# Kernel optimization log

Measured on AMD Instinct MI355X. Metric: run time of the kernel, lower is better.

## Reference

```python
import jax, jax.numpy as jnp
import numpy as np

N = 50000
E = 800000
EP = 200000
IN_C = 128
HID = 128


def setup_inputs() -> dict:
    key = jax.random.key(0)
    ks = jax.random.split(key, 10)
    x = jax.random.normal(ks[0], (N, IN_C), dtype=jnp.float32)
    edge_index = jax.random.randint(ks[1], (2, E), 0, N, dtype=jnp.int64)
    pred_edges = jax.random.randint(ks[2], (2, EP), 0, N, dtype=jnp.int64)
    s_in = 1.0 / np.sqrt(IN_C)
    s_h = 1.0 / np.sqrt(HID)
    W1l = jax.random.normal(ks[3], (IN_C, HID), dtype=jnp.float32) * s_in
    W1r = jax.random.normal(ks[4], (IN_C, HID), dtype=jnp.float32) * s_in
    b1 = jnp.zeros((HID,), dtype=jnp.float32)
    W2l = jax.random.normal(ks[5], (HID, HID), dtype=jnp.float32) * s_h
    W2r = jax.random.normal(ks[6], (HID, HID), dtype=jnp.float32) * s_h
    b2 = jnp.zeros((HID,), dtype=jnp.float32)
    return {"x": x, "W1l": W1l, "b1": b1, "W1r": W1r,
            "W2l": W2l, "b2": b2, "W2r": W2r,
            "edge_index": edge_index, "pred_edges": pred_edges}


def _sage_conv(h, Wl, b, Wr, src, dst, n_nodes):
    # PyG SAGEConv (aggr='mean'): out = lin_l(mean_j x_j) + lin_r(x_i)
    msg = h[src]                                              # (E, D) gather
    agg = jax.ops.segment_sum(msg, dst, num_segments=n_nodes)  # (N, D) scatter-add
    deg = jax.ops.segment_sum(jnp.ones((src.shape[0],), h.dtype), dst,
                              num_segments=n_nodes)
    agg = agg / jnp.maximum(deg, 1.0)[:, None]                # mean (0 for isolated)
    return agg @ Wl + b + h @ Wr


def reference(x, W1l, b1, W1r, W2l, b2, W2r, edge_index, pred_edges):
    n_nodes = x.shape[0]
    src, dst = edge_index[0], edge_index[1]
    h = jax.nn.relu(_sage_conv(x, W1l, b1, W1r, src, dst, n_nodes))
    z = _sage_conv(h, W2l, b2, W2r, src, dst, n_nodes)
    ps, pd = pred_edges[0], pred_edges[1]
    return jnp.sum(z[ps] * z[pd], axis=-1)  # (E_pred,) logits
```

## Files before the change

### kernel.cpp

```cpp
#include <hip/hip_runtime.h>

#define D 128

typedef __attribute__((ext_vector_type(8))) short short8;
typedef __attribute__((ext_vector_type(4))) float f32x4;

__device__ inline unsigned int f2bf_bits(float f) {
    unsigned int u = __float_as_uint(f);
    return (u + 0x7FFFu + ((u >> 16) & 1u)) >> 16;
}

__device__ inline float bfhi(unsigned int u) { return __uint_as_float(u << 16); }
__device__ inline float bflo(unsigned int u) { return __uint_as_float(u & 0xffff0000u); }

__global__ __launch_bounds__(256) void prep_kernel(
    const float* __restrict__ x,
    const float* __restrict__ W1l, const float* __restrict__ W1r,
    const float* __restrict__ W2l, const float* __restrict__ W2r,
    unsigned short* __restrict__ xbf, unsigned short* __restrict__ xlo,
    unsigned short* __restrict__ h1, unsigned short* __restrict__ l1,
    unsigned short* __restrict__ h2, unsigned short* __restrict__ l2,
    int n4, int ncast, int* __restrict__ chist, int* __restrict__ csrpad)
{
    const int b = blockIdx.x;
    const int t = threadIdx.x;
    if (b < ncast) {
        int i = b * 256 + t;
        if (i >= n4) return;
        f32x4 v = *(const f32x4*)(x + (size_t)i * 4);
        ushort4 oh, ol;
        {
            unsigned int h; float hf;
            h = f2bf_bits(v.x); hf = __uint_as_float(h << 16);
            oh.x = (unsigned short)h; ol.x = (unsigned short)f2bf_bits(v.x - hf);
            h = f2bf_bits(v.y); hf = __uint_as_float(h << 16);
            oh.y = (unsigned short)h; ol.y = (unsigned short)f2bf_bits(v.y - hf);
            h = f2bf_bits(v.z); hf = __uint_as_float(h << 16);
            oh.z = (unsigned short)h; ol.z = (unsigned short)f2bf_bits(v.z - hf);
            h = f2bf_bits(v.w); hf = __uint_as_float(h << 16);
            oh.w = (unsigned short)h; ol.w = (unsigned short)f2bf_bits(v.w - hf);
        }
        *(ushort4*)(xbf + (size_t)i * 4) = oh;
        *(ushort4*)(xlo + (size_t)i * 4) = ol;
    } else if (b < ncast + 256) {
        int gidx = (b - ncast) * 256 + t;
        int sel = gidx >> 15;
        int idx = gidx & 32767;
        int tt = idx >> 12;
        int ks = (idx >> 9) & 7;
        int lane = (idx >> 3) & 63;
        int j = idx & 7;
        int qq = lane >> 4, r16 = lane & 15;
        int k = ks * 32 + qq * 8 + j;
        int c = tt * 16 + r16;
        const float* Wl = sel ? W2l : W1l;
        const float* Wr = sel ? W2r : W1r;
        float v = (k < 128) ? Wl[k * 128 + c] : Wr[(k - 128) * 128 + c];
        unsigned int h = f2bf_bits(v);
        float hf = __uint_as_float(h << 16);
        unsigned int l = f2bf_bits(v - hf);
        (sel ? h2 : h1)[idx] = (unsigned short)h;
        (sel ? l2 : l1)[idx] = (unsigned short)l;
    } else {
        chist[t] = 0;
        if (t < 16) csrpad[t] = 0;
    }
}

__global__ __launch_bounds__(256) void coarse_count_kernel(const int* __restrict__ dst,
                                                           int* __restrict__ chist, int E) {
    __shared__ int h[256];
    h[threadIdx.x] = 0;
    __syncthreads();
    const int stride = gridDim.x * 256;
    for (int e = blockIdx.x * 256 + threadIdx.x; e < E; e += stride)
        atomicAdd(&h[dst[e] >> 8], 1);
    __syncthreads();
    int v = h[threadIdx.x];
    if (v) atomicAdd(&chist[threadIdx.x], v);
}

__global__ __launch_bounds__(256) void scan256_kernel(const int* __restrict__ chist,
                                                      int* __restrict__ cbase,
                                                      int* __restrict__ gcur) {
    __shared__ int wsum[4];
    const int t = threadIdx.x, lane = t & 63, wv = t >> 6;
    int v = chist[t];
    int s = v;
#pragma unroll
    for (int o = 1; o < 64; o <<= 1) {
        int u = __shfl_up(s, o, 64);
        if (lane >= o) s += u;
    }
    if (lane == 63) wsum[wv] = s;
    __syncthreads();
    int add = 0;
    for (int w = 0; w < wv; ++w) add += wsum[w];
    cbase[t + 1] = s + add;
    if (t == 0) cbase[0] = 0;
    gcur[t] = s + add - v;
}

#define CCHUNK 4096
__global__ __launch_bounds__(256) void coarse_scatter_kernel(
    const int* __restrict__ src, const int* __restrict__ dst,
    int* __restrict__ gcur, unsigned int* __restrict__ centries, int E)
{
    __shared__ int h[256];
    __shared__ int base[256];
    __shared__ unsigned int stage[CCHUNK];
    const int t = threadIdx.x;
    const int e0 = blockIdx.x * CCHUNK;
    h[t] = 0;
    __syncthreads();
#pragma unroll
    for (int i = 0; i < 16; ++i) {
        int e = e0 + i * 256 + t;
        unsigned int u = 0xFFFFFFFFu;
        if (e < E) {
            int d = dst[e];
            int s = src[e];
            int b = d >> 8;
            u = ((unsigned)b << 24) | ((unsigned)s << 8) | (unsigned)(d & 255);
            atomicAdd(&h[b], 1);
        }
        stage[i * 256 + t] = u;
    }
    __syncthreads();
    base[t] = atomicAdd(&gcur[t], h[t]);
    __syncthreads();
    h[t] = 0;
    __syncthreads();
#pragma unroll
    for (int i = 0; i < 16; ++i) {
        unsigned int u = stage[i * 256 + t];
        if (u != 0xFFFFFFFFu) {
            int b = u >> 24;
            int r = atomicAdd(&h[b], 1);
            centries[base[b] + r] = u & 0x00FFFFFFu;
        }
    }
}

#define DCAP 8192
__global__ __launch_bounds__(256) void fine_bucket_kernel(
    const unsigned int* __restrict__ centries,
    const int* __restrict__ cbase,
    int* __restrict__ offo, int* __restrict__ csr, int N, int E)
{
    __shared__ int h[256], ex[256], wsum[4];
    __shared__ int stg[DCAP];
    const int t = threadIdx.x, lane = t & 63, wv = t >> 6;
    const int b = blockIdx.x;
    const int s0 = cbase[b];
    const int cnt = cbase[b + 1] - s0;
    h[t] = 0;
    __syncthreads();
    for (int i = t; i < cnt; i += 256)
        atomicAdd(&h[centries[s0 + i] & 255], 1);
    __syncthreads();
    int v = h[t], s = v;
#pragma unroll
    for (int o = 1; o < 64; o <<= 1) {
        int u = __shfl_up(s, o, 64);
        if (lane >= o) s += u;
    }
    if (lane == 63) wsum[wv] = s;
    __syncthreads();
    int add = 0;
    for (int w = 0; w < wv; ++w) add += wsum[w];
    const int exc = s + add - v;
    ex[t] = exc;
    const int dg = b * 256 + t;
    if (dg < N) offo[dg] = s0 + exc;
    if (b == 0 && t == 0) offo[N] = E;
    h[t] = 0;
    __syncthreads();
    if (cnt <= DCAP) {
        for (int i = t; i < cnt; i += 256) {
            unsigned int u = centries[s0 + i];
            int dl = u & 255;
            int r = atomicAdd(&h[dl], 1);
            stg[ex[dl] + r] = (int)(u >> 8);
        }
        __syncthreads();
        for (int i = t; i < cnt; i += 256)
            csr[s0 + i] = stg[i];
    } else {
        for (int i = t; i < cnt; i += 256) {
            unsigned int u = centries[s0 + i];
            int dl = u & 255;
            int r = atomicAdd(&h[dl], 1);
            csr[s0 + ex[dl] + r] = (int)(u >> 8);
        }
    }
}

__device__ inline void loadb8(const unsigned short* __restrict__ bh,
                              const unsigned short* __restrict__ bl,
                              int ks, short8* BH, short8* BL) {
    const unsigned short* p = bh + (size_t)ks * 512;
    const unsigned short* q = bl + (size_t)ks * 512;
#pragma unroll
    for (int t = 0; t < 8; ++t) {
        BH[t] = *(const short8*)(p + (size_t)t * 4096);
        BL[t] = *(const short8*)(q + (size_t)t * 4096);
    }
}

__device__ inline void mfma24(const short8& AH, const short8& AL,
                              const short8* BH, const short8* BL, f32x4* acc) {
#pragma unroll
    for (int t = 0; t < 8; ++t) {
        acc[t] = __builtin_amdgcn_mfma_f32_16x16x32_bf16(AH, BH[t], acc[t], 0, 0, 0);
        acc[t] = __builtin_amdgcn_mfma_f32_16x16x32_bf16(AL, BH[t], acc[t], 0, 0, 0);
        acc[t] = __builtin_amdgcn_mfma_f32_16x16x32_bf16(AH, BL[t], acc[t], 0, 0, 0);
    }
}

__global__ __launch_bounds__(64, 3) void fused_sage_kernel(
    const unsigned short* __restrict__ featbf,
    const int* __restrict__ off,
    const int* __restrict__ csr,
    const unsigned short* __restrict__ self_hi,
    const unsigned short* __restrict__ self_lo,
    const unsigned short* __restrict__ wpk_hi,
    const unsigned short* __restrict__ wpk_lo,
    const float* __restrict__ bias,
    unsigned short* __restrict__ out_hi,
    unsigned short* __restrict__ out_lo,
    int do_relu)
{
    const int lane = threadIdx.x;
    const int tile = blockIdx.x;
    const int q = lane >> 4, r16 = lane & 15;
    const int n0w = tile * 16;
    const int node = n0w + r16;

    const unsigned short* bh = wpk_hi + lane * 8;
    const unsigned short* bl = wpk_lo + lane * 8;

    short8 BH0[8], BL0[8], BH1[8], BL1[8];
    loadb8(bh, bl, 0, BH0, BL0);

    const int start = off[node];
    const int end   = off[node + 1];
    const unsigned short* fb = featbf + q * 8;
    float ga[4][8];
#pragma unroll
    for (int k = 0; k < 4; ++k)
#pragma unroll
        for (int c = 0; c < 8; ++c) ga[k][c] = 0.f;

#define ACCUM(rv, k)                                                     \
    { ga[k][0] += bfhi(rv.x); ga[k][1] += bflo(rv.x);                    \
      ga[k][2] += bfhi(rv.y); ga[k][3] += bflo(rv.y);                    \
      ga[k][4] += bfhi(rv.z); ga[k][5] += bflo(rv.z);                    \
      ga[k][6] += bfhi(rv.w); ga[k][7] += bflo(rv.w); }

    const uint4 zero4 = {0u, 0u, 0u, 0u};
    if (start < end) {
        int4 ix = *(const int4*)(csr + start);
        for (int e = start; e < end; e += 4) {
            int4 ixn = *(const int4*)(csr + e + 4);
            const unsigned short* p0 = fb + (size_t)ix.x * D;
            const unsigned short* p1 = fb + (size_t)ix.y * D;
            const unsigned short* p2 = fb + (size_t)ix.z * D;
            const unsigned short* p3 = fb + (size_t)ix.w * D;
            uint4 r00 = *(const uint4*)(p0);
            uint4 r01 = *(const uint4*)(p0 + 32);
            uint4 r02 = *(const uint4*)(p0 + 64);
            uint4 r03 = *(const uint4*)(p0 + 96);
            uint4 r10 = *(const uint4*)(p1);
            uint4 r11 = *(const uint4*)(p1 + 32);
            uint4 r12 = *(const uint4*)(p1 + 64);
            uint4 r13 = *(const uint4*)(p1 + 96);
            uint4 r20 = *(const uint4*)(p2);
            uint4 r21 = *(const uint4*)(p2 + 32);
            uint4 r22 = *(const uint4*)(p2 + 64);
            uint4 r23 = *(const uint4*)(p2 + 96);
            uint4 r30 = *(const uint4*)(p3);
            uint4 r31 = *(const uint4*)(p3 + 32);
            uint4 r32 = *(const uint4*)(p3 + 64);
            uint4 r33 = *(const uint4*)(p3 + 96);
            if (e + 1 >= end) { r10 = zero4; r11 = zero4; r12 = zero4; r13 = zero4; }
            if (e + 2 >= end) { r20 = zero4; r21 = zero4; r22 = zero4; r23 = zero4; }
            if (e + 3 >= end) { r30 = zero4; r31 = zero4; r32 = zero4; r33 = zero4; }
            ACCUM(r00, 0) ACCUM(r01, 1) ACCUM(r02, 2) ACCUM(r03, 3)
            ACCUM(r10, 0) ACCUM(r11, 1) ACCUM(r12, 2) ACCUM(r13, 3)
            ACCUM(r20, 0) ACCUM(r21, 1) ACCUM(r22, 2) ACCUM(r23, 3)
            ACCUM(r30, 0) ACCUM(r31, 1) ACCUM(r32, 2) ACCUM(r33, 3)
            ix = ixn;
        }
    }
#undef ACCUM

    const float dinv = 1.0f / (float)max(end - start, 1);
    short8 AH[4], AL[4];
#pragma unroll
    for (int k = 0; k < 4; ++k) {
#pragma unroll
        for (int c = 0; c < 8; ++c) {
            float v = ga[k][c] * dinv;
            unsigned int hbits = f2bf_bits(v);
            AH[k][c] = (short)hbits;
            AL[k][c] = (short)f2bf_bits(v - __uint_as_float(hbits << 16));
        }
    }

    f32x4 acc8[8];
#pragma unroll
    for (int t = 0; t < 8; ++t) acc8[t] = (f32x4){0.f, 0.f, 0.f, 0.f};

    const unsigned short* sph = self_hi + (size_t)node * D + q * 8;
    const unsigned short* spl = self_lo + (size_t)node * D + q * 8;

    short8 SH0, SL0, SH1, SL1;
    loadb8(bh, bl, 1, BH1, BL1);
    SH0 = *(const short8*)(sph);
    SL0 = *(const short8*)(spl);
    mfma24(AH[0], AL[0], BH0, BL0, acc8);
    loadb8(bh, bl, 2, BH0, BL0);
    SH1 = *(const short8*)(sph + 32);
    SL1 = *(const short8*)(spl + 32);
    mfma24(AH[1], AL[1], BH1, BL1, acc8);
    loadb8(bh, bl, 3, BH1, BL1);
    mfma24(AH[2], AL[2], BH0, BL0, acc8);
    loadb8(bh, bl, 4, BH0, BL0);
    mfma24(AH[3], AL[3], BH1, BL1, acc8);
    loadb8(bh, bl, 5, BH1, BL1);
    mfma24(SH0, SL0, BH0, BL0, acc8);
    loadb8(bh, bl, 6, BH0, BL0);
    SH0 = *(const short8*)(sph + 64);
    SL0 = *(const short8*)(spl + 64);
    mfma24(SH1, SL1, BH1, BL1, acc8);
    loadb8(bh, bl, 7, BH1, BL1);
    SH1 = *(const short8*)(sph + 96);
    SL1 = *(const short8*)(spl + 96);
    mfma24(SH0, SL0, BH0, BL0, acc8);
    mfma24(SH1, SL1, BH1, BL1, acc8);

#pragma unroll
    for (int t = 0; t < 8; ++t) {
        const float bv = bias[t * 16 + r16];
#pragma unroll
        for (int r = 0; r < 4; ++r) {
            float vv = acc8[t][r] + bv;
            if (do_relu) vv = fmaxf(vv, 0.f);
            const size_t o = (size_t)(n0w + q * 4 + r) * D + t * 16 + r16;
            unsigned int h = f2bf_bits(vv);
            out_hi[o] = (unsigned short)h;
            if (out_lo) {
                float hf = __uint_as_float(h << 16);
                out_lo[o] = (unsigned short)f2bf_bits(vv - hf);
            }
        }
    }
}

__global__ __launch_bounds__(256) void pred_kernel(const unsigned short* __restrict__ zbf,
                                                   const int* __restrict__ ps,
                                                   const int* __restrict__ pd,
                                                   float* __restrict__ out, int EP) {
    int idx = blockIdx.x * blockDim.x + threadIdx.x;
    int e = idx >> 5;
    if (e >= EP) return;
    int l = idx & 31;
    const unsigned short* fb = zbf + (size_t)l * 4;
    uint2 ra = *(const uint2*)(fb + (size_t)ps[e] * D);
    uint2 rb = *(const uint2*)(fb + (size_t)pd[e] * D);
    float p = __uint_as_float(ra.x << 16)         * __uint_as_float(rb.x << 16)
            + __uint_as_float(ra.x & 0xffff0000u) * __uint_as_float(rb.x & 0xffff0000u)
            + __uint_as_float(ra.y << 16)         * __uint_as_float(rb.y << 16)
            + __uint_as_float(ra.y & 0xffff0000u) * __uint_as_float(rb.y & 0xffff0000u);
#pragma unroll
    for (int off = 16; off > 0; off >>= 1) p += __shfl_xor(p, off, 32);
    if (l == 0) out[e] = p;
}

extern "C" void kernel_launch(void* const* d_in, const int* in_sizes, int n_in,
                              void* d_out, int out_size, void* d_ws, size_t ws_size,
                              hipStream_t stream) {
    const float* x   = (const float*)d_in[0];
    const float* W1l = (const float*)d_in[1];
    const float* b1  = (const float*)d_in[2];
    const float* W1r = (const float*)d_in[3];
    const float* W2l = (const float*)d_in[4];
    const float* b2  = (const float*)d_in[5];
    const float* W2r = (const float*)d_in[6];
    const int* edge_index = (const int*)d_in[7];
    const int* pred_edges = (const int*)d_in[8];
    float* out = (float*)d_out;

    const int N  = in_sizes[0] / D;
    const int E  = in_sizes[7] / 2;
    const int EP = in_sizes[8] / 2;

    const int* src = edge_index;
    const int* dst = edge_index + E;
    const int* ps  = pred_edges;
    const int* pd  = pred_edges + EP;

    int* chist   = (int*)d_ws;
    int* cbase   = chist + 256;
    int* gcur    = cbase + 272;
    int* off     = gcur + 256;
    unsigned int* centries = (unsigned int*)(off + 50016);
    int* csr     = (int*)(centries + E);
    unsigned short* w1_hi = (unsigned short*)(csr + E + 16);
    unsigned short* w1_lo = w1_hi + 32768;
    unsigned short* w2_hi = w1_lo + 32768;
    unsigned short* w2_lo = w2_hi + 32768;
    unsigned short* xbf   = w2_lo + 32768;
    unsigned short* xlo   = xbf + (size_t)N * D;
    unsigned short* hbf   = xlo + (size_t)N * D;
    unsigned short* hlo   = hbf + (size_t)N * D;
    unsigned short* zbf   = hlo + (size_t)N * D;

    const int n4 = N * D / 4;
    const int ncast = (n4 + 255) / 256;
    const int ntiles = N / 16;
    const int nbC = (E + CCHUNK - 1) / CCHUNK;
    const int nbD = (N + 255) / 256;
    const int nblk_pred = (EP * 32 + 255) / 256;

    prep_kernel<<<ncast + 257, 256, 0, stream>>>(x, W1l, W1r, W2l, W2r,
                                                 xbf, xlo, w1_hi, w1_lo, w2_hi, w2_lo,
                                                 n4, ncast, chist, csr + E);

    coarse_count_kernel<<<256, 256, 0, stream>>>(dst, chist, E);
    scan256_kernel<<<1, 256, 0, stream>>>(chist, cbase, gcur);
    coarse_scatter_kernel<<<nbC, 256, 0, stream>>>(src, dst, gcur, centries, E);
    fine_bucket_kernel<<<nbD, 256, 0, stream>>>(centries, cbase, off, csr, N, E);

    fused_sage_kernel<<<ntiles, 64, 0, stream>>>(xbf, off, csr, xbf, xlo,
                                                 w1_hi, w1_lo, b1, hbf, hlo, 1);
    fused_sage_kernel<<<ntiles, 64, 0, stream>>>(hbf, off, csr, hbf, hlo,
                                                 w2_hi, w2_lo, b2, zbf,
                                                 (unsigned short*)nullptr, 0);
    pred_kernel<<<nblk_pred, 256, 0, stream>>>(zbf, ps, pd, out, EP);
}
```

Baseline: 299.2 us.

## Split SAGE tile across four waves with LDS-shared aggregates and coalesced stores

The fused SAGE kernel moves from one 64-thread wave per 16-node tile to four waves. Each wave gathers and averages a 32-column slice of the neighbour features, and the gather now prefetches the next four neighbour rows while accumulating the current ones. The bf16 hi/lo aggregates are exchanged through shared memory, so each wave computes 32 output columns with MFMA instead of all 128. Outputs are staged in shared memory and written back as coalesced 16-byte stores. The aim is to cut per-thread register pressure and raise memory-level parallelism on the gather. The cost is two block-wide barriers and extra shared-memory traffic.

```diff
diff --git a/kernel.cpp b/kernel.cpp
--- a/kernel.cpp
+++ b/kernel.cpp
@@ -196,29 +196,7 @@
     }
 }
 
-__device__ inline void loadb8(const unsigned short* __restrict__ bh,
-                              const unsigned short* __restrict__ bl,
-                              int ks, short8* BH, short8* BL) {
-    const unsigned short* p = bh + (size_t)ks * 512;
-    const unsigned short* q = bl + (size_t)ks * 512;
-#pragma unroll
-    for (int t = 0; t < 8; ++t) {
-        BH[t] = *(const short8*)(p + (size_t)t * 4096);
-        BL[t] = *(const short8*)(q + (size_t)t * 4096);
-    }
-}
-
-__device__ inline void mfma24(const short8& AH, const short8& AL,
-                              const short8* BH, const short8* BL, f32x4* acc) {
-#pragma unroll
-    for (int t = 0; t < 8; ++t) {
-        acc[t] = __builtin_amdgcn_mfma_f32_16x16x32_bf16(AH, BH[t], acc[t], 0, 0, 0);
-        acc[t] = __builtin_amdgcn_mfma_f32_16x16x32_bf16(AL, BH[t], acc[t], 0, 0, 0);
-        acc[t] = __builtin_amdgcn_mfma_f32_16x16x32_bf16(AH, BL[t], acc[t], 0, 0, 0);
-    }
-}
-
-__global__ __launch_bounds__(64, 3) void fused_sage_kernel(
+__global__ __launch_bounds__(256, 4) void fused_sage_kernel(
     const unsigned short* __restrict__ featbf,
     const int* __restrict__ off,
     const int* __restrict__ csr,
@@ -231,129 +209,126 @@
     unsigned short* __restrict__ out_lo,
     int do_relu)
 {
-    const int lane = threadIdx.x;
+    __shared__ unsigned short AHs[4][64][8];
+    __shared__ unsigned short ALs[4][64][8];
+    __shared__ unsigned short outs_hi[16][128];
+    __shared__ unsigned short outs_lo[16][128];
+
+    const int w = threadIdx.x >> 6;
+    const int l = threadIdx.x & 63;
     const int tile = blockIdx.x;
-    const int q = lane >> 4, r16 = lane & 15;
     const int n0w = tile * 16;
-    const int node = n0w + r16;
-
-    const unsigned short* bh = wpk_hi + lane * 8;
-    const unsigned short* bl = wpk_lo + lane * 8;
-
-    short8 BH0[8], BL0[8], BH1[8], BL1[8];
-    loadb8(bh, bl, 0, BH0, BL0);
-
-    const int start = off[node];
-    const int end   = off[node + 1];
-    const unsigned short* fb = featbf + q * 8;
-    float ga[4][8];
-#pragma unroll
-    for (int k = 0; k < 4; ++k)
-#pragma unroll
-        for (int c = 0; c < 8; ++c) ga[k][c] = 0.f;
-
-#define ACCUM(rv, k)                                                     \
-    { ga[k][0] += bfhi(rv.x); ga[k][1] += bflo(rv.x);                    \
-      ga[k][2] += bfhi(rv.y); ga[k][3] += bflo(rv.y);                    \
-      ga[k][4] += bfhi(rv.z); ga[k][5] += bflo(rv.z);                    \
-      ga[k][6] += bfhi(rv.w); ga[k][7] += bflo(rv.w); }
+
+    const int gn = l >> 2;
+    const int q2 = l & 3;
+    const int gnode = n0w + gn;
+    const int start = off[gnode];
+    const int end   = off[gnode + 1];
+    const unsigned short* fb = featbf + w * 32 + q2 * 8;
+
+    float ga[8] = {0.f, 0.f, 0.f, 0.f, 0.f, 0.f, 0.f, 0.f};
+
+#define ACC(rv)                                                         \
+    { ga[0] += bfhi(rv.x); ga[1] += bflo(rv.x);                         \
+      ga[2] += bfhi(rv.y); ga[3] += bflo(rv.y);                         \
+      ga[4] += bfhi(rv.z); ga[5] += bflo(rv.z);                         \
+      ga[6] += bfhi(rv.w); ga[7] += bflo(rv.w); }
 
     const uint4 zero4 = {0u, 0u, 0u, 0u};
     if (start < end) {
         int4 ix = *(const int4*)(csr + start);
+        uint4 c0 = *(const uint4*)(fb + (size_t)ix.x * D);
+        uint4 c1 = *(const uint4*)(fb + (size_t)ix.y * D);
+        uint4 c2 = *(const uint4*)(fb + (size_t)ix.z * D);
+        uint4 c3 = *(const uint4*)(fb + (size_t)ix.w * D);
         for (int e = start; e < end; e += 4) {
             int4 ixn = *(const int4*)(csr + e + 4);
-            const unsigned short* p0 = fb + (size_t)ix.x * D;
-            const unsigned short* p1 = fb + (size_t)ix.y * D;
-            const unsigned short* p2 = fb + (size_t)ix.z * D;
-            const unsigned short* p3 = fb + (size_t)ix.w * D;
-            uint4 r00 = *(const uint4*)(p0);
-            uint4 r01 = *(const uint4*)(p0 + 32);
-            uint4 r02 = *(const uint4*)(p0 + 64);
-            uint4 r03 = *(const uint4*)(p0 + 96);
-            uint4 r10 = *(const uint4*)(p1);
-            uint4 r11 = *(const uint4*)(p1 + 32);
-            uint4 r12 = *(const uint4*)(p1 + 64);
-            uint4 r13 = *(const uint4*)(p1 + 96);
-            uint4 r20 = *(const uint4*)(p2);
-            uint4 r21 = *(const uint4*)(p2 + 32);
-            uint4 r22 = *(const uint4*)(p2 + 64);
-            uint4 r23 = *(const uint4*)(p2 + 96);
-            uint4 r30 = *(const uint4*)(p3);
-            uint4 r31 = *(const uint4*)(p3 + 32);
-            uint4 r32 = *(const uint4*)(p3 + 64);
-            uint4 r33 = *(const uint4*)(p3 + 96);
-            if (e + 1 >= end) { r10 = zero4; r11 = zero4; r12 = zero4; r13 = zero4; }
-            if (e + 2 >= end) { r20 = zero4; r21 = zero4; r22 = zero4; r23 = zero4; }
-            if (e + 3 >= end) { r30 = zero4; r31 = zero4; r32 = zero4; r33 = zero4; }
-            ACCUM(r00, 0) ACCUM(r01, 1) ACCUM(r02, 2) ACCUM(r03, 3)
-            ACCUM(r10, 0) ACCUM(r11, 1) ACCUM(r12, 2) ACCUM(r13, 3)
-            ACCUM(r20, 0) ACCUM(r21, 1) ACCUM(r22, 2) ACCUM(r23, 3)
-            ACCUM(r30, 0) ACCUM(r31, 1) ACCUM(r32, 2) ACCUM(r33, 3)
-            ix = ixn;
-        }
-    }
-#undef ACCUM
-
-    const float dinv = 1.0f / (float)max(end - start, 1);
-    short8 AH[4], AL[4];
-#pragma unroll
-    for (int k = 0; k < 4; ++k) {
+            uint4 n0 = *(const uint4*)(fb + (size_t)ixn.x * D);
+            uint4 n1 = *(const uint4*)(fb + (size_t)ixn.y * D);
+            uint4 n2 = *(const uint4*)(fb + (size_t)ixn.z * D);
+            uint4 n3 = *(const uint4*)(fb + (size_t)ixn.w * D);
+            if (e + 1 >= end) c1 = zero4;
+            if (e + 2 >= end) c2 = zero4;
+            if (e + 3 >= end) c3 = zero4;
+            ACC(c0) ACC(c1) ACC(c2) ACC(c3)
+            c0 = n0; c1 = n1; c2 = n2; c3 = n3;
+        }
+    }
+#undef ACC
+
+    {
+        const float dinv = 1.0f / (float)max(end - start, 1);
+        short8 hi8, lo8;
 #pragma unroll
         for (int c = 0; c < 8; ++c) {
-            float v = ga[k][c] * dinv;
-            unsigned int hbits = f2bf_bits(v);
-            AH[k][c] = (short)hbits;
-            AL[k][c] = (short)f2bf_bits(v - __uint_as_float(hbits << 16));
-        }
-    }
-
-    f32x4 acc8[8];
-#pragma unroll
-    for (int t = 0; t < 8; ++t) acc8[t] = (f32x4){0.f, 0.f, 0.f, 0.f};
-
-    const unsigned short* sph = self_hi + (size_t)node * D + q * 8;
-    const unsigned short* spl = self_lo + (size_t)node * D + q * 8;
-
-    short8 SH0, SL0, SH1, SL1;
-    loadb8(bh, bl, 1, BH1, BL1);
-    SH0 = *(const short8*)(sph);
-    SL0 = *(const short8*)(spl);
-    mfma24(AH[0], AL[0], BH0, BL0, acc8);
-    loadb8(bh, bl, 2, BH0, BL0);
-    SH1 = *(const short8*)(sph + 32);
-    SL1 = *(const short8*)(spl + 32);
-    mfma24(AH[1], AL[1], BH1, BL1, acc8);
-    loadb8(bh, bl, 3, BH1, BL1);
-    mfma24(AH[2], AL[2], BH0, BL0, acc8);
-    loadb8(bh, bl, 4, BH0, BL0);
-    mfma24(AH[3], AL[3], BH1, BL1, acc8);
-    loadb8(bh, bl, 5, BH1, BL1);
-    mfma24(SH0, SL0, BH0, BL0, acc8);
-    loadb8(bh, bl, 6, BH0, BL0);
-    SH0 = *(const short8*)(sph + 64);
-    SL0 = *(const short8*)(spl + 64);
-    mfma24(SH1, SL1, BH1, BL1, acc8);
-    loadb8(bh, bl, 7, BH1, BL1);
-    SH1 = *(const short8*)(sph + 96);
-    SL1 = *(const short8*)(spl + 96);
-    mfma24(SH0, SL0, BH0, BL0, acc8);
-    mfma24(SH1, SL1, BH1, BL1, acc8);
-
-#pragma unroll
-    for (int t = 0; t < 8; ++t) {
-        const float bv = bias[t * 16 + r16];
+            float v = ga[c] * dinv;
+            unsigned int hb = f2bf_bits(v);
+            hi8[c] = (short)hb;
+            lo8[c] = (short)f2bf_bits(v - __uint_as_float(hb << 16));
+        }
+        *(short8*)&AHs[w][q2 * 16 + gn][0] = hi8;
+        *(short8*)&ALs[w][q2 * 16 + gn][0] = lo8;
+    }
+    __syncthreads();
+
+    const int q = l >> 4, r16 = l & 15;
+    const int mnode = n0w + r16;
+    f32x4 acc0 = {0.f, 0.f, 0.f, 0.f};
+    f32x4 acc1 = {0.f, 0.f, 0.f, 0.f};
+    const unsigned short* sph = self_hi + (size_t)mnode * D + q * 8;
+    const unsigned short* spl = self_lo + (size_t)mnode * D + q * 8;
+    const unsigned short* bh0 = wpk_hi + (size_t)(2 * w) * 4096 + l * 8;
+    const unsigned short* bl0 = wpk_lo + (size_t)(2 * w) * 4096 + l * 8;
+
+#pragma unroll
+    for (int ks = 0; ks < 8; ++ks) {
+        short8 AH, AL;
+        if (ks < 4) {
+            AH = *(const short8*)&AHs[ks][l][0];
+            AL = *(const short8*)&ALs[ks][l][0];
+        } else {
+            AH = *(const short8*)(sph + (ks - 4) * 32);
+            AL = *(const short8*)(spl + (ks - 4) * 32);
+        }
+        short8 BH0 = *(const short8*)(bh0 + ks * 512);
+        short8 BL0 = *(const short8*)(bl0 + ks * 512);
+        short8 BH1 = *(const short8*)(bh0 + 4096 + ks * 512);
+        short8 BL1 = *(const short8*)(bl0 + 4096 + ks * 512);
+        acc0 = __builtin_amdgcn_mfma_f32_16x16x32_bf16(AH, BH0, acc0, 0, 0, 0);
+        acc0 = __builtin_amdgcn_mfma_f32_16x16x32_bf16(AL, BH0, acc0, 0, 0, 0);
+        acc0 = __builtin_amdgcn_mfma_f32_16x16x32_bf16(AH, BL0, acc0, 0, 0, 0);
+        acc1 = __builtin_amdgcn_mfma_f32_16x16x32_bf16(AH, BH1, acc1, 0, 0, 0);
+        acc1 = __builtin_amdgcn_mfma_f32_16x16x32_bf16(AL, BH1, acc1, 0, 0, 0);
+        acc1 = __builtin_amdgcn_mfma_f32_16x16x32_bf16(AH, BL1, acc1, 0, 0, 0);
+    }
+
+    {
+        const float bv0 = bias[32 * w + r16];
+        const float bv1 = bias[32 * w + 16 + r16];
 #pragma unroll
         for (int r = 0; r < 4; ++r) {
-            float vv = acc8[t][r] + bv;
-            if (do_relu) vv = fmaxf(vv, 0.f);
-            const size_t o = (size_t)(n0w + q * 4 + r) * D + t * 16 + r16;
-            unsigned int h = f2bf_bits(vv);
-            out_hi[o] = (unsigned short)h;
-            if (out_lo) {
-                float hf = __uint_as_float(h << 16);
-                out_lo[o] = (unsigned short)f2bf_bits(vv - hf);
-            }
+            float v0 = acc0[r] + bv0;
+            float v1 = acc1[r] + bv1;
+            if (do_relu) { v0 = fmaxf(v0, 0.f); v1 = fmaxf(v1, 0.f); }
+            const int row = q * 4 + r;
+            unsigned int h0 = f2bf_bits(v0);
+            unsigned int h1 = f2bf_bits(v1);
+            outs_hi[row][32 * w + r16] = (unsigned short)h0;
+            outs_hi[row][32 * w + 16 + r16] = (unsigned short)h1;
+            outs_lo[row][32 * w + r16] =
+                (unsigned short)f2bf_bits(v0 - __uint_as_float(h0 << 16));
+            outs_lo[row][32 * w + 16 + r16] =
+                (unsigned short)f2bf_bits(v1 - __uint_as_float(h1 << 16));
+        }
+    }
+    __syncthreads();
+    {
+        const int tid = threadIdx.x;
+        short8 vh = *(short8*)(&outs_hi[0][0] + tid * 8);
+        *(short8*)(out_hi + (size_t)n0w * D + tid * 8) = vh;
+        if (out_lo) {
+            short8 vl = *(short8*)(&outs_lo[0][0] + tid * 8);
+            *(short8*)(out_lo + (size_t)n0w * D + tid * 8) = vl;
         }
     }
 }
@@ -433,10 +408,10 @@
     coarse_scatter_kernel<<<nbC, 256, 0, stream>>>(src, dst, gcur, centries, E);
     fine_bucket_kernel<<<nbD, 256, 0, stream>>>(centries, cbase, off, csr, N, E);
 
-    fused_sage_kernel<<<ntiles, 64, 0, stream>>>(xbf, off, csr, xbf, xlo,
-                                                 w1_hi, w1_lo, b1, hbf, hlo, 1);
-    fused_sage_kernel<<<ntiles, 64, 0, stream>>>(hbf, off, csr, hbf, hlo,
-                                                 w2_hi, w2_lo, b2, zbf,
-                                                 (unsigned short*)nullptr, 0);
+    fused_sage_kernel<<<ntiles, 256, 0, stream>>>(xbf, off, csr, xbf, xlo,
+                                                  w1_hi, w1_lo, b1, hbf, hlo, 1);
+    fused_sage_kernel<<<ntiles, 256, 0, stream>>>(hbf, off, csr, hbf, hlo,
+                                                  w2_hi, w2_lo, b2, zbf,
+                                                  (unsigned short*)nullptr, 0);
     pred_kernel<<<nblk_pred, 256, 0, stream>>>(zbf, ps, pd, out, EP);
 }
```

After: 247.3 us. 17.3% less time.
